# Optimization experiments

Measured on AMD Instinct MI355X. Metric: run time of the kernel, lower is better.

## Reference

```python
import jax, jax.numpy as jnp
import numpy as np

H, W, V = 32, 64, 13
B, C_IN = 8, 256
RADIUS = 6371.0 * 1000.0
NUM_LAT = H + 2
_j = np.arange(1, NUM_LAT - 1, dtype=np.float64)
_LATS = (90.0 - _j * 180.0 / (NUM_LAT - 1)) * np.pi / 180.0  # [32] radians
PIXEL_X = jnp.asarray(2.0 * np.pi * RADIUS * np.cos(_LATS) / W, dtype=jnp.float32).reshape(1, 1, H, 1)
PIXEL_Y = np.float32(np.pi * RADIUS / (H + 1))
_DZ = np.array([50, 50, 50, 50, 50, 75, 100, 100, 100, 125, 112, 75, 75], dtype=np.float32)
PIXEL_Z = jnp.asarray(_DZ).reshape(1, V, 1, 1)
PRESSURE = jnp.asarray([50, 100, 150, 200, 250, 300, 400, 500, 600, 700, 850, 925, 1000], dtype=jnp.float32).reshape(1, V, 1, 1)
M_Z = jnp.asarray(np.tril(np.ones((V, V), dtype=np.float32)) * _DZ[None, :])  # lower-tri integration matrix
LAT_GRID = jnp.asarray(_LATS, dtype=jnp.float32).reshape(1, 1, H, 1)

OMEGA, L_V, R_GAS, C_P, R_D = 7.29e-5, 2.5e6, 8.314, 1005.0, 287.0
DIFF_RATIO, DT, K_H, K_V = 0.05, 300.0, 15.0, 0.1
SIGMA, EMIS, PTHRESH = 5.67e-8, 0.7, 0.8
sg = jax.lax.stop_gradient


def d_x(f):  # periodic 4th-order diff along W, kernel [1,-8,0,8,-1]/12
    g = (jnp.roll(f, 2, 3) - 8.0 * jnp.roll(f, 1, 3) + 8.0 * jnp.roll(f, -1, 3) - jnp.roll(f, -2, 3)) / 12.0
    return g / PIXEL_X


def d_y(f):  # replicate-block padding along H, kernel [-1,8,0,-8,1]/12
    p = jnp.concatenate([f[:, :, :2], f, f[:, :, -2:]], axis=2)
    g = (-p[:, :, :-4] + 8.0 * p[:, :, 1:-3] - 8.0 * p[:, :, 3:-1] + p[:, :, 4:]) / 12.0
    return g / PIXEL_Y


def d_z(f):  # replicate-block padding along level dim (axis 1)
    p = jnp.concatenate([f[:, :2], f, f[:, -2:]], axis=1)
    g = (-p[:, :-4] + 8.0 * p[:, 1:-3] - 8.0 * p[:, 3:-1] + p[:, 4:]) / 12.0
    return g / PIXEL_Z


def integral_z(f):
    return jnp.einsum('ij,bjhw->bihw', M_Z, f)


def conv3x3(x, w, b):
    y = jax.lax.conv_general_dilated(x, w, (1, 1), ((1, 1), (1, 1)), dimension_numbers=('NCHW', 'OIHW', 'NCHW'))
    return y + b[None, :, None, None]


def batchnorm(x, g, b, eps=1e-5):  # training-mode BN (batch statistics)
    m = x.mean(axis=(0, 2, 3), keepdims=True)
    v = x.var(axis=(0, 2, 3), keepdims=True)
    return (x - m) / jnp.sqrt(v + eps) * g.reshape(1, -1, 1, 1) + b.reshape(1, -1, 1, 1)


def scale_tensor(t, a, b):
    mn, mx = sg(t.min()), sg(t.max())
    return (t - mn) / (mx - mn) * (b - a) + a


def scale_diff(d, x):
    mn, me, mx = sg(x.min()), sg(x.mean()), sg(x.max())
    return scale_tensor(d, (mn - me) * DIFF_RATIO, (mx - me) * DIFF_RATIO)


def avoid_inf(t, thr=1.0):
    t = jnp.where(jnp.abs(t) == 0.0, jnp.full_like(t, 0.1), t)
    return jnp.where(jnp.abs(t) < thr, jnp.sign(t) * thr, t)


def mixing(f):
    return K_H * (d_x(d_x(f)) + d_y(d_y(f))) + K_V * d_z(d_z(f))


def rad_cool(t):
    ta = t + 273.15
    return -(EMIS * SIGMA * ta ** 4) / (C_P * PRESSURE * 100.0 / (R_D * ta))


def saturation(t, z_z):
    rho = -1.0 / avoid_inf(z_z)
    p = rho * R_GAS * t
    tc = t - 273.15
    e_s = 6.112 * jnp.exp(scale_tensor(17.67 * tc / avoid_inf(tc + 243.5), -3.47, 3.01)) * 100.0
    return jnp.maximum(0.622 * e_s / avoid_inf(p - 0.378 * e_s), 1e-6)


def precip(q, q_s):
    rh = q / avoid_inf(q_s)
    rate = (rh > PTHRESH).astype(q.dtype) * (q - PTHRESH * q_s) / DT
    return rate, rate * L_V / C_P


def uv_dt(u, v, w, u_x, v_y, z_x, z_y):
    # u_x, v_y are held fixed across RK stages (stateful self.u_x/self.v_y in the original)
    f_cor = 2.0 * OMEGA * jnp.sin(LAT_GRID)
    u_t = -u * u_x - v * d_y(u) - w * d_z(u) + f_cor * v - z_x + mixing(u)
    v_t = -u * d_x(v) - v * v_y - w * d_z(v) - f_cor * u - z_y + mixing(v)
    return u_t, v_t


def t_dt(u, v, w, t, q, q_s, z_z):
    Q = -L_V * z_z * w
    _, lh = precip(q, q_s)
    return (Q - z_z * w) / C_P - u * d_x(t) - v * d_y(t) - w * d_z(t) + mixing(t) + rad_cool(t) + lh


def pde_forward(x, w_norm, b_norm, w_innorm, b_innorm, coef, gz, bz, gq, bq, gu, bu, gv, bv, gt, bt, gblk, bblk):
    h = conv3x3(x, w_norm, b_norm)  # [B, 65, H, W]
    z, q, u, v, t = jnp.split(h, 5, axis=1)
    z = batchnorm(z, gz, bz); q = batchnorm(q, gq, bq)
    u = batchnorm(u, gu, bu); v = batchnorm(v, gv, bv); t = batchnorm(t, gt, bt)
    z_x, z_y, z_z = d_x(z), d_y(z), d_z(z)
    u_x, v_y = d_x(u), d_y(v)
    w_vel = -integral_z(u_x + v_y)  # continuity: dw/dz = -(u_x + v_y)
    # --- RK4 momentum evolution ---
    k1u, k1v = uv_dt(u, v, w_vel, u_x, v_y, z_x, z_y)
    k2u, k2v = uv_dt(u + 0.5 * DT * k1u, v + 0.5 * DT * k1v, w_vel, u_x, v_y, z_x, z_y)
    k3u, k3v = uv_dt(u + 0.5 * DT * k2u, v + 0.5 * DT * k2v, w_vel, u_x, v_y, z_x, z_y)
    k4u, k4v = uv_dt(u + DT * k3u, v + DT * k3v, w_vel, u_x, v_y, z_x, z_y)
    u_new = u + sg(scale_diff((k1u + 2 * k2u + 2 * k3u + k4u) / 6.0 * DT, u))
    v_new = v + sg(scale_diff((k1v + 2 * k2v + 2 * k3v + k4v) / 6.0 * DT, v))
    # --- RK4 temperature evolution (q_s fixed from initial t) ---
    q_s = saturation(t, z_z)
    k1t = t_dt(u, v, w_vel, t, q, q_s, z_z)
    k2t = t_dt(u, v, w_vel, t + 0.5 * DT * k1t, q, q_s, z_z)
    k3t = t_dt(u, v, w_vel, t + 0.5 * DT * k2t, q, q_s, z_z)
    k4t = t_dt(u, v, w_vel, t + DT * k3t, q, q_s, z_z)
    t_new = t + sg(scale_diff((k1t + 2 * k2t + 2 * k3t + k4t) / 6.0 * DT, t))
    # geopotential tendency uses stateful self.t_t (last computed stage = k4t)
    z_t = integral_z(-R_GAS / PRESSURE * k4t)
    z_new = z + sg(scale_diff(z_t * DT, z))
    # moisture evolution
    pr, _ = precip(q, q_s)
    q_t = -u * d_x(q) - v * d_y(q) - w_vel * d_z(q) + mixing(q) - pr
    q_new = q + sg(scale_diff(q_t * DT, q))
    phys = jnp.concatenate([z_new, q_new, u_new, v_new, t_new], axis=1)
    out = coef * phys + (1.0 - coef) * h
    out = conv3x3(out, w_innorm, b_innorm)
    return batchnorm(out, gblk, bblk) + x


def setup_inputs() -> dict:
    key = jax.random.key(0)
    k0, k1, k2 = jax.random.split(key, 3)
    VD = V * 5
    ones13 = jnp.ones((V,), jnp.float32)
    zeros13 = jnp.zeros((V,), jnp.float32)
    return {
        'x': jax.random.normal(k0, (B, C_IN, H, W), jnp.float32),
        'w_norm': jax.random.normal(k1, (VD, C_IN, 3, 3), jnp.float32) * 0.02,
        'b_norm': jnp.zeros((VD,), jnp.float32),
        'w_innorm': jax.random.normal(k2, (C_IN, VD, 3, 3), jnp.float32) * 0.02,
        'b_innorm': jnp.zeros((C_IN,), jnp.float32),
        'coef': 0.5 * jnp.ones((1, VD, H, W), jnp.float32),
        'gz': 0.1 * ones13, 'bz': zeros13,
        'gq': 0.1 * ones13, 'bq': zeros13,
        'gu': 0.1 * ones13, 'bu': zeros13,
        'gv': 0.1 * ones13, 'bv': zeros13,
        'gt': 0.1 * ones13, 'bt': zeros13,
        'gblk': jnp.ones((C_IN,), jnp.float32),
        'bblk': jnp.zeros((C_IN,), jnp.float32),
    }


def reference(x, w_norm, b_norm, w_innorm, b_innorm, coef, gz, bz, gq, bq, gu, bu, gv, bv, gt, bt, gblk, bblk):
    return pde_forward(x, w_norm, b_norm, w_innorm, b_innorm, coef, gz, bz, gq, bq, gu, bu, gv, bv, gt, bt, gblk, bblk)
```

## Files before the change

### kernel.cpp

```cpp
#include <hip/hip_runtime.h>
#include <math.h>

#define DEVFN static __device__ __forceinline__

static constexpr int BB = 8, VV = 13, HH = 32, WW = 64;
static constexpr int NPLANE = HH * WW;
static constexpr int NF = BB * VV * NPLANE;
static constexpr int NHB = BB * 65 * NPLANE;

static constexpr float DT = 300.0f;
static constexpr float KHc = 15.0f, KVc = 0.1f;
static constexpr float OMEGAc = 7.29e-5f;
static constexpr float L_Vc = 2.5e6f;
static constexpr float R_GASc = 8.314f;
static constexpr float C_Pc = 1005.0f;
static constexpr float PTHc = 0.8f;
static constexpr float PYc  = (float)(3.14159265358979323846 * 6371000.0 / 33.0);
static constexpr float PXCc = (float)(2.0 * 3.14159265358979323846 * 6371000.0 / 64.0);
static constexpr float RCCc = (float)(0.7 * 5.67e-8 * 287.0 / (1005.0 * 100.0));
static constexpr float FBIG = 3.402823466e38f;

__constant__ float cDZ[13]  = {50,50,50,50,50,75,100,100,100,125,112,75,75};
__constant__ float cPRS[13] = {50,100,150,200,250,300,400,500,600,700,850,925,1000};

typedef short bf16x8 __attribute__((ext_vector_type(8)));
typedef float f32x4 __attribute__((ext_vector_type(4)));

DEVFN int pmh(int r){ return r < 0 ? r + 2 : (r > HH - 1 ? r - 2 : r); }
DEVFN int pmv(int r){ return r < 0 ? r + 2 : (r > VV - 1 ? r - 2 : r); }
DEVFN float latOf(int h){ return (90.0f - (float)(h + 1) * (180.0f / 33.0f)) * 0.017453292519943295f; }
DEVFN float avoid_inf(float t){
  if (t == 0.0f) t = 0.1f;
  if (fabsf(t) < 1.0f) t = copysignf(1.0f, t);
  return t;
}
DEVFN unsigned short f2bf(float f){
  unsigned u = __float_as_uint(f);
  unsigned r = (u + 0x7fffu + ((u >> 16) & 1u)) >> 16;
  return (unsigned short)r;
}

DEVFN float d_xf(const float* __restrict__ F, int rb, int w, float invpx){
  return (F[rb + ((w + 62) & 63)] - 8.f * F[rb + ((w + 63) & 63)]
        + 8.f * F[rb + ((w + 1) & 63)] - F[rb + ((w + 2) & 63)]) * (1.f / 12.f) * invpx;
}
DEVFN float d_yf(const float* __restrict__ F, int bvbase, int h, int w){
  return (-F[bvbase + pmh(h - 2) * 64 + w] + 8.f * F[bvbase + pmh(h - 1) * 64 + w]
          - 8.f * F[bvbase + pmh(h + 1) * 64 + w] + F[bvbase + pmh(h + 2) * 64 + w]) * (1.f / 12.f) * (1.f / PYc);
}
DEVFN float d_zf(const float* __restrict__ F, int bbase, int v, int hw){
  return (-F[bbase + pmv(v - 2) * 2048 + hw] + 8.f * F[bbase + pmv(v - 1) * 2048 + hw]
          - 8.f * F[bbase + pmv(v + 1) * 2048 + hw] + F[bbase + pmv(v + 2) * 2048 + hw]) * (1.f / 12.f) / cDZ[v];
}
DEVFN float dxxf(const float* __restrict__ F, int rb, int w, float invpx){
  float s = F[rb + ((w + 60) & 63)] - 16.f * F[rb + ((w + 61) & 63)] + 64.f * F[rb + ((w + 62) & 63)]
          + 16.f * F[rb + ((w + 63) & 63)] - 130.f * F[rb + w] + 16.f * F[rb + ((w + 1) & 63)]
          + 64.f * F[rb + ((w + 2) & 63)] - 16.f * F[rb + ((w + 3) & 63)] + F[rb + ((w + 4) & 63)];
  return s * (1.f / 144.f) * invpx * invpx;
}
DEVFN float dyyf(const float* __restrict__ F, int bvbase, int h, int w){
  float g0 = d_yf(F, bvbase, pmh(h - 2), w);
  float g1 = d_yf(F, bvbase, pmh(h - 1), w);
  float g2 = d_yf(F, bvbase, pmh(h + 1), w);
  float g3 = d_yf(F, bvbase, pmh(h + 2), w);
  return (-g0 + 8.f * g1 - 8.f * g2 + g3) * (1.f / 12.f) * (1.f / PYc);
}
DEVFN float dzzf(const float* __restrict__ F, int bbase, int v, int hw){
  float g0 = d_zf(F, bbase, pmv(v - 2), hw);
  float g1 = d_zf(F, bbase, pmv(v - 1), hw);
  float g2 = d_zf(F, bbase, pmv(v + 1), hw);
  float g3 = d_zf(F, bbase, pmv(v + 2), hw);
  return (-g0 + 8.f * g1 - 8.f * g2 + g3) * (1.f / 12.f) / cDZ[v];
}

DEVFN float waveRedSum(float v){ for (int o = 32; o; o >>= 1) v += __shfl_down(v, o, 64); return v; }
DEVFN float waveRedMin(float v){ for (int o = 32; o; o >>= 1) v = fminf(v, __shfl_down(v, o, 64)); return v; }
DEVFN float waveRedMax(float v){ for (int o = 32; o; o >>= 1) v = fmaxf(v, __shfl_down(v, o, 64)); return v; }

template<int OP, int NWV>
static __device__ float blockRedN(float v){
  __shared__ float s[NWV];
  v = OP == 0 ? waveRedSum(v) : OP == 1 ? waveRedMin(v) : waveRedMax(v);
  int lane = threadIdx.x & 63, wid = threadIdx.x >> 6;
  __syncthreads();
  if (lane == 0) s[wid] = v;
  __syncthreads();
  float r = s[0];
  #pragma unroll
  for (int k = 1; k < NWV; ++k)
    r = OP == 0 ? r + s[k] : OP == 1 ? fminf(r, s[k]) : fmaxf(r, s[k]);
  return r;
}

struct GB { const float* g[5]; const float* b[5]; };

__global__ void __launch_bounds__(256) pre_k(const float* __restrict__ x,
    const float* __restrict__ w1, const float* __restrict__ w2,
    unsigned short* __restrict__ XT, unsigned short* __restrict__ wp1,
    unsigned short* __restrict__ wp2)
{
  int blk = blockIdx.x, t = threadIdx.x;
  if (blk < 1024){
    __shared__ float tile[16 * 68];
    int zz = blk >> 8, rem = blk & 255;
    int b = rem >> 5, h = rem & 31;
    for (int p = zz * 4; p < zz * 4 + 4; ++p){
      int cbase = p * 16;
      __syncthreads();
      {
        int cl = t >> 4, w4 = (t & 15) * 4;
        float4 v = *(const float4*)(x + (((size_t)(b * 256 + cbase + cl) * 32 + h) * 64 + w4));
        tile[cl * 68 + w4 + 0] = v.x; tile[cl * 68 + w4 + 1] = v.y;
        tile[cl * 68 + w4 + 2] = v.z; tile[cl * 68 + w4 + 3] = v.w;
      }
      __syncthreads();
      {
        int w = t >> 2, c4 = (t & 3) * 4;
        ushort4 o;
        o.x = f2bf(tile[(c4 + 0) * 68 + w]);
        o.y = f2bf(tile[(c4 + 1) * 68 + w]);
        o.z = f2bf(tile[(c4 + 2) * 68 + w]);
        o.w = f2bf(tile[(c4 + 3) * 68 + w]);
        *(ushort4*)(XT + (((size_t)(b * 32 + h) * 64 + w) * 256 + cbase + c4)) = o;
      }
    }
  } else {
    const int T1 = 9 * 80 * 256;
    const int T2 = 9 * 256 * 96;
    int idx = (blk - 1024) * 256 + t;
    if (idx < T1){
      int dir = idx / (80 * 256);
      int r = idx - dir * (80 * 256);
      int co = r / 256, ci = r - co * 256;
      float v = (co < 65) ? w1[((size_t)(co * 256 + ci)) * 9 + dir] : 0.f;
      wp1[idx] = f2bf(v);
    } else if (idx < T1 + T2){
      int j = idx - T1;
      int dir = j / (256 * 96);
      int r = j - dir * (256 * 96);
      int co = r / 96, ci = r - co * 96;
      float v = (ci < 65) ? w2[((size_t)(co * 65 + ci)) * 9 + dir] : 0.f;
      wp2[j] = f2bf(v);
    }
  }
}

template<int CIT, int CIL, int CO, int COp, int NW, int MF, int SWZ>
__global__ void __launch_bounds__(NW * 64) conv_mfma_k(
    const unsigned short* __restrict__ XT, const unsigned short* __restrict__ Wp,
    const float* __restrict__ bias, float* __restrict__ out, float* __restrict__ bnp)
{
  __shared__ __align__(16) unsigned short Xl[3 * 34 * CIL];
  const int C8 = CIL / 8;
  int tid = threadIdx.x;
  int bx = blockIdx.x, b = blockIdx.y;
  int h = bx >> 1, p0 = (bx & 1) << 5;
  int bh = b * 64 + bx;
  int wid = tid >> 6, lane = tid & 63;
  int l15 = lane & 15, q = lane >> 4;

  f32x4 acc[MF][2];
  #pragma unroll
  for (int mf = 0; mf < MF; ++mf)
    #pragma unroll
    for (int nf = 0; nf < 2; ++nf){ f32x4 z = {0.f, 0.f, 0.f, 0.f}; acc[mf][nf] = z; }

  for (int cp = 0; cp < CIT / CIL; ++cp){
    if (cp) __syncthreads();
    for (int idx = tid; idx < 3 * 34 * C8; idx += NW * 64){
      int r = idx / (34 * C8);
      int rest = idx - r * (34 * C8);
      int j = rest / C8;
      int c8 = rest - j * C8;
      int hh = h + r - 1;
      int gw = p0 - 1 + j;
      uint4 val = make_uint4(0, 0, 0, 0);
      if (hh >= 0 && hh < 32 && gw >= 0 && gw < 64)
        val = *(const uint4*)(XT + (((size_t)(b * 32 + hh) * 64 + gw) * CIT + cp * CIL + c8 * 8));
      int dst = (r * 34 + j) * CIL + ((c8 * 8) ^ ((j & SWZ) << 3));
      *(uint4*)(Xl + dst) = val;
    }
    __syncthreads();

    for (int dir = 0; dir < 9; ++dir){
      int dy = dir / 3, dx = dir - dy * 3;
      #pragma unroll
      for (int kc = 0; kc < CIL / 32; ++kc){
        int kb = kc * 32 + q * 8;
        bf16x8 a[MF];
        #pragma unroll
        for (int mf = 0; mf < MF; ++mf){
          int co = wid * (MF * 16) + mf * 16 + l15;
          a[mf] = *(const bf16x8*)(Wp + ((size_t)(dir * COp + co) * CIT + cp * CIL + kb));
        }
        #pragma unroll
        for (int nf = 0; nf < 2; ++nf){
          int j = nf * 16 + l15 + dx;
          bf16x8 bfrag = *(const bf16x8*)(Xl + ((dy * 34 + j) * CIL + (kb ^ ((j & SWZ) << 3))));
          #pragma unroll
          for (int mf = 0; mf < MF; ++mf)
            acc[mf][nf] = __builtin_amdgcn_mfma_f32_16x16x32_bf16(a[mf], bfrag, acc[mf][nf], 0, 0, 0);
        }
      }
    }
  }
  #pragma unroll
  for (int mf = 0; mf < MF; ++mf){
    #pragma unroll
    for (int r = 0; r < 4; ++r){
      int co = wid * (MF * 16) + mf * 16 + q * 4 + r;
      if (CO != COp && co >= CO) continue;
      float bv = bias[co];
      float sv = 0.f, sq = 0.f;
      #pragma unroll
      for (int nf = 0; nf < 2; ++nf){
        int pix = nf * 16 + l15;
        float val = acc[mf][nf][r] + bv;
        out[(size_t)(b * CO + co) * 2048 + h * 64 + p0 + pix] = val;
        sv += val; sq += val * val;
      }
      #pragma unroll
      for (int off = 8; off; off >>= 1){
        sv += __shfl_xor(sv, off, 16);
        sq += __shfl_xor(sq, off, 16);
      }
      if (l15 == 0){
        bnp[((size_t)co * 512 + bh) * 2]     = sv;
        bnp[((size_t)co * 512 + bh) * 2 + 1] = sq;
      }
    }
  }
}

__global__ void __launch_bounds__(256) prep_k(const float* __restrict__ hb,
  const float* __restrict__ bnp1, GB gb,
  float* __restrict__ Fz, float* __restrict__ Fq, float* __restrict__ Fu,
  float* __restrict__ Fvf, float* __restrict__ Ft,
  float* __restrict__ zx, float* __restrict__ zy, float* __restrict__ zz,
  float* __restrict__ ux, float* __restrict__ vy, float* __restrict__ wv,
  float* __restrict__ partS)
{
  __shared__ float As[65], Bs[65];
  int blk = blockIdx.x, t = threadIdx.x;
  {
    int wvid = t >> 6, lane = t & 63;
    for (int ch = wvid; ch < 65; ch += 4){
      const float4* pp = (const float4*)(bnp1 + (size_t)ch * 1024) + lane * 4;
      float s = 0.f, sq = 0.f;
      #pragma unroll
      for (int k = 0; k < 4; ++k){ float4 v = pp[k]; s += v.x + v.z; sq += v.y + v.w; }
      s = waveRedSum(s); sq = waveRedSum(sq);
      if (!lane){
        float m = s * (1.f / 16384.f);
        float var = sq * (1.f / 16384.f) - m * m;
        float rstd = rsqrtf(var + 1e-5f);
        int f = ch / 13, k = ch - f * 13;
        float g = gb.g[f][k], bbv = gb.b[f][k];
        As[ch] = g * rstd; Bs[ch] = bbv - m * g * rstd;
      }
    }
  }
  __syncthreads();

  int part = blk >> 6;
  int col = ((blk & 63) << 8) | t;
  int b = col >> 11, p = col & 2047, h = p >> 6, w = p & 63;
  int hbase = b * 65 * NPLANE;
  auto hn = [&](int ch, int hh, int ww)->float {
    return hb[hbase + ch * 2048 + hh * 64 + ww] * As[ch] + Bs[ch];
  };
  int fb = (b * 13) * 2048 + p;
  float lat = latOf(h);
  float invpx = 1.0f / (PXCc * cosf(lat));
  int wm2 = (w + 62) & 63, wm1 = (w + 63) & 63, wpl1 = (w + 1) & 63, wpl2 = (w + 2) & 63;
  int hm2 = pmh(h - 2), hm1 = pmh(h - 1), hp1 = pmh(h + 1), hp2 = pmh(h + 2);
  float fmn = FBIG, fmx = -FBIG, fsm = 0.f, smn = FBIG, smx = -FBIG;
  if (part < 5){
    int ch0 = part * 13;
    float c[13];
    #pragma unroll
    for (int v = 0; v < 13; ++v) c[v] = hn(ch0 + v, h, w);
    float* Fdst = part == 0 ? Fz : part == 1 ? Fq : part == 2 ? Fu : part == 3 ? Fvf : Ft;
    #pragma unroll
    for (int v = 0; v < 13; ++v) Fdst[fb + v * 2048] = c[v];
    if (part == 0){
      #pragma unroll
      for (int v = 0; v < 13; ++v){
        zz[fb + v * 2048] = (-c[pmv(v - 2)] + 8.f * c[pmv(v - 1)] - 8.f * c[pmv(v + 1)] + c[pmv(v + 2)]) * (1.f / 12.f) / cDZ[v];
        float zxv = (hn(v, h, wm2) - 8.f * hn(v, h, wm1) + 8.f * hn(v, h, wpl1) - hn(v, h, wpl2)) * (1.f / 12.f) * invpx;
        float zyv = (-hn(v, hm2, w) + 8.f * hn(v, hm1, w) - 8.f * hn(v, hp1, w) + hn(v, hp2, w)) * (1.f / 12.f) * (1.f / PYc);
        zx[fb + v * 2048] = zxv; zy[fb + v * 2048] = zyv;
      }
    }
    if (part == 2){
      #pragma unroll
      for (int v = 0; v < 13; ++v){
        float uxv = (hn(26 + v, h, wm2) - 8.f * hn(26 + v, h, wm1) + 8.f * hn(26 + v, h, wpl1) - hn(26 + v, h, wpl2)) * (1.f / 12.f) * invpx;
        ux[fb + v * 2048] = uxv;
      }
    }
    if (part == 3){
      #pragma unroll
      for (int v = 0; v < 13; ++v){
        float vyv = (-hn(39 + v, hm2, w) + 8.f * hn(39 + v, hm1, w) - 8.f * hn(39 + v, hp1, w) + hn(39 + v, hp2, w)) * (1.f / 12.f) * (1.f / PYc);
        vy[fb + v * 2048] = vyv;
      }
    }
    if (part == 4){
      #pragma unroll
      for (int v = 0; v < 13; ++v){
        float tcc = c[v] - 273.15f;
        float arg = 17.67f * tcc / avoid_inf(tcc + 243.5f);
        smn = fminf(smn, arg); smx = fmaxf(smx, arg);
      }
    }
    #pragma unroll
    for (int v = 0; v < 13; ++v){ fmn = fminf(fmn, c[v]); fmx = fmaxf(fmx, c[v]); fsm += c[v]; }
  } else {
    float cum = 0.f;
    #pragma unroll
    for (int v = 0; v < 13; ++v){
      float uxv = (hn(26 + v, h, wm2) - 8.f * hn(26 + v, h, wm1) + 8.f * hn(26 + v, h, wpl1) - hn(26 + v, h, wpl2)) * (1.f / 12.f) * invpx;
      float vyv = (-hn(39 + v, hm2, w) + 8.f * hn(39 + v, hm1, w) - 8.f * hn(39 + v, hp1, w) + hn(39 + v, hp2, w)) * (1.f / 12.f) * (1.f / PYc);
      cum += cDZ[v] * (uxv + vyv);
      wv[fb + v * 2048] = -cum;
    }
  }
  float* pb = partS + blk * 17;
  float r;
  r = blockRedN<1,4>(smn); if (!t) pb[0] = r;
  r = blockRedN<2,4>(smx); if (!t) pb[1] = r;
  #pragma unroll
  for (int f = 0; f < 5; ++f){
    r = blockRedN<1,4>(part == f ? fmn : FBIG);  if (!t) pb[2 + f * 3] = r;
    r = blockRedN<2,4>(part == f ? fmx : -FBIG); if (!t) pb[3 + f * 3] = r;
    r = blockRedN<0,4>(part == f ? fsm : 0.f);   if (!t) pb[4 + f * 3] = r;
  }
}

template<int STAGE>
__global__ void __launch_bounds__(256) stage_k(
  const float* U, const float* Vf, const float* T,
  const float* Fu, const float* Fvf, const float* Ft, const float* Fq,
  const float* ux, const float* vy, const float* zx, const float* zy,
  const float* wv, const float* zz, const float* partS,
  float* C0, float* prr,
  float* Uo, float* Vo, float* To,
  float* duA, float* dvA, float* dtA, float* k4t, float* qtA,
  float* pduv, float* pdt, float* pqt, float cnext)
{
  float ss = 0.f, off = 0.f;
  if (STAGE == 1){
    int tt = threadIdx.x;
    float v0 = partS[tt * 17], v1 = partS[tt * 17 + 1];
    if (tt < 128){
      v0 = fminf(v0, partS[(tt + 256) * 17]);
      v1 = fmaxf(v1, partS[(tt + 256) * 17 + 1]);
    }
    float smn = blockRedN<1,4>(v0);
    float smx = blockRedN<2,4>(v1);
    ss = (3.01f + 3.47f) / (smx - smn);
    off = -3.47f - smn * ss;
  }
  int i = blockIdx.x * 256 + threadIdx.x;
  int w = i & 63, h = (i >> 6) & 31;
  int bv = i >> 11;
  int v = bv % 13;
  int bvbase = bv * 2048;
  int rb = bvbase + h * 64;
  int bbase = (bv - v) * 2048;
  int hw = h * 64 + w;
  float lat = latOf(h);
  float invpx = 1.0f / (PXCc * cosf(lat));
  float fcor = 2.0f * OMEGAc * sinf(lat);
  float wvi = wv[i];
  float Ui = U[i], Vi = Vf[i], Ti = T[i];
  float Fui = (STAGE == 1) ? Ui : Fu[i];
  float Fvi = (STAGE == 1) ? Vi : Fvf[i];

  float dyU = d_yf(U, bvbase, h, w);
  float dzU = d_zf(U, bbase, v, hw);
  float dxV = d_xf(Vf, rb, w, invpx);
  float dzV = d_zf(Vf, bbase, v, hw);
  float mixU = KHc * (dxxf(U, rb, w, invpx) + dyyf(U, bvbase, h, w)) + KVc * dzzf(U, bbase, v, hw);
  float mixV = KHc * (dxxf(Vf, rb, w, invpx) + dyyf(Vf, bvbase, h, w)) + KVc * dzzf(Vf, bbase, v, hw);
  float ku = -Ui * ux[i] - Vi * dyU - wvi * dzU + fcor * Vi - zx[i] + mixU;
  float kv = -Ui * dxV - Vi * vy[i] - wvi * dzV - fcor * Ui - zy[i] + mixV;

  float C0i;
  if (STAGE == 1){
    float zzi = zz[i], qi = Fq[i];
    float rho = -1.0f / avoid_inf(zzi);
    float p = rho * R_GASc * Ti;
    float tcc = Ti - 273.15f;
    float arg = 17.67f * tcc / avoid_inf(tcc + 243.5f);
    float es = 6.112f * expf(arg * ss + off) * 100.0f;
    float qs = fmaxf(0.622f * es / avoid_inf(p - 0.378f * es), 1e-6f);
    float rh = qi / avoid_inf(qs);
    float rate = (rh > PTHc) ? (qi - PTHc * qs) * (1.0f / DT) : 0.0f;
    prr[i] = rate;
    C0i = -(L_Vc + 1.0f) * zzi * wvi * (1.0f / C_Pc) + rate * (L_Vc / C_Pc);
    C0[i] = C0i;
  } else {
    C0i = C0[i];
  }

  float dxT = d_xf(T, rb, w, invpx);
  float dyT = d_yf(T, bvbase, h, w);
  float dzT = d_zf(T, bbase, v, hw);
  float mixT = KHc * (dxxf(T, rb, w, invpx) + dyyf(T, bvbase, h, w)) + KVc * dzzf(T, bbase, v, hw);
  float ta = Ti + 273.15f;
  float t2 = ta * ta;
  float ta5 = t2 * t2 * ta;
  float rc = -RCCc * ta5 / cPRS[v];
  float kt = C0i - Fui * dxT - Fvi * dyT - wvi * dzT + mixT + rc;

  if (STAGE == 1){ duA[i] = ku; dvA[i] = kv; dtA[i] = kt; }
  else if (STAGE < 4){ duA[i] += 2.f * ku; dvA[i] += 2.f * kv; dtA[i] += 2.f * kt; }
  else {
    float au = duA[i] + ku, av = dvA[i] + kv, at = dtA[i] + kt;
    duA[i] = au; dvA[i] = av; dtA[i] = at; k4t[i] = kt;
    float m0 = blockRedN<1,4>(au), m1 = blockRedN<2,4>(au);
    float m2 = blockRedN<1,4>(av), m3 = blockRedN<2,4>(av);
    float m4 = blockRedN<1,4>(at), m5 = blockRedN<2,4>(at);
    if (!threadIdx.x){
      float* pp = pduv + blockIdx.x * 4;
      pp[0] = m0; pp[1] = m1; pp[2] = m2; pp[3] = m3;
      pdt[blockIdx.x * 2] = m4; pdt[blockIdx.x * 2 + 1] = m5;
    }
  }
  if (STAGE < 4){
    float Fti = (STAGE == 1) ? Ti : Ft[i];
    Uo[i] = Fui + cnext * ku;
    Vo[i] = Fvi + cnext * kv;
    To[i] = Fti + cnext * kt;
  }

  if (STAGE == 2){
    float qtv = -Fui * d_xf(Fq, rb, w, invpx) - Fvi * d_yf(Fq, bvbase, h, w) - wvi * d_zf(Fq, bbase, v, hw)
              + KHc * (dxxf(Fq, rb, w, invpx) + dyyf(Fq, bvbase, h, w)) + KVc * dzzf(Fq, bbase, v, hw) - prr[i];
    qtA[i] = qtv;
    float m0 = blockRedN<1,4>(qtv), m1 = blockRedN<2,4>(qtv);
    if (!threadIdx.x){ pqt[blockIdx.x * 2] = m0; pqt[blockIdx.x * 2 + 1] = m1; }
  }
}

__global__ void __launch_bounds__(64) zt_k(const float* __restrict__ k4t, float* __restrict__ zt, float* __restrict__ pmm)
{
  int col = blockIdx.x * 64 + threadIdx.x;
  int b = col >> 11, p = col & 2047;
  int fb = b * 13 * 2048 + p;
  float cum = 0.f, mn = FBIG, mx = -FBIG;
  #pragma unroll
  for (int v = 0; v < 13; ++v){
    cum += cDZ[v] * (-R_GASc / cPRS[v]) * k4t[fb + v * 2048];
    zt[fb + v * 2048] = cum;
    mn = fminf(mn, cum); mx = fmaxf(mx, cum);
  }
  mn = waveRedMin(mn); mx = waveRedMax(mx);
  if (!threadIdx.x){ pmm[blockIdx.x * 2] = mn; pmm[blockIdx.x * 2 + 1] = mx; }
}

__global__ void __launch_bounds__(256) outmid_fused_k(
  const float* __restrict__ hb,
  const float* __restrict__ Fz, const float* __restrict__ Fq, const float* __restrict__ Fu,
  const float* __restrict__ Fvf, const float* __restrict__ Ft,
  const float* __restrict__ ztA, const float* __restrict__ qtA,
  const float* __restrict__ duA, const float* __restrict__ dvA, const float* __restrict__ dtA,
  const float* __restrict__ coef, const float* __restrict__ partS,
  const float* __restrict__ pduv, const float* __restrict__ pdt,
  const float* __restrict__ pqt, const float* __restrict__ pzt,
  unsigned short* __restrict__ MT)
{
  __shared__ float tileBig[65 * 66];
  int blk = blockIdx.x, t = threadIdx.x;

  float fmn[5] = {FBIG, FBIG, FBIG, FBIG, FBIG};
  float fmx[5] = {-FBIG, -FBIG, -FBIG, -FBIG, -FBIG};
  float fsm[5] = {0.f, 0.f, 0.f, 0.f, 0.f};
  #pragma unroll 1
  for (int r0 = t; r0 < 384; r0 += 256){
    const float* pr = partS + r0 * 17;
    #pragma unroll
    for (int f = 0; f < 5; ++f){
      fmn[f] = fminf(fmn[f], pr[2 + f * 3]);
      fmx[f] = fmaxf(fmx[f], pr[3 + f * 3]);
      fsm[f] += pr[4 + f * 3];
    }
  }
  #pragma unroll
  for (int f = 0; f < 5; ++f){
    fmn[f] = blockRedN<1,4>(fmn[f]);
    fmx[f] = blockRedN<2,4>(fmx[f]);
    fsm[f] = blockRedN<0,4>(fsm[f]);
  }
  float dumn = FBIG, dumx = -FBIG, dvmn = FBIG, dvmx = -FBIG, dtmn = FBIG, dtmx = -FBIG;
  float qmn = FBIG, qmx = -FBIG;
  #pragma unroll 1
  for (int r0 = t; r0 < 832; r0 += 256){
    dumn = fminf(dumn, pduv[r0 * 4]);     dumx = fmaxf(dumx, pduv[r0 * 4 + 1]);
    dvmn = fminf(dvmn, pduv[r0 * 4 + 2]); dvmx = fmaxf(dvmx, pduv[r0 * 4 + 3]);
    dtmn = fminf(dtmn, pdt[r0 * 2]);      dtmx = fmaxf(dtmx, pdt[r0 * 2 + 1]);
    qmn = fminf(qmn, pqt[r0 * 2]);        qmx = fmaxf(qmx, pqt[r0 * 2 + 1]);
  }
  float zmn = pzt[t * 2], zmx = pzt[t * 2 + 1];
  dumn = blockRedN<1,4>(dumn); dumx = blockRedN<2,4>(dumx);
  dvmn = blockRedN<1,4>(dvmn); dvmx = blockRedN<2,4>(dvmx);
  dtmn = blockRedN<1,4>(dtmn); dtmx = blockRedN<2,4>(dtmx);
  qmn = blockRedN<1,4>(qmn);   qmx = blockRedN<2,4>(qmx);
  zmn = blockRedN<1,4>(zmn);   zmx = blockRedN<2,4>(zmx);

  float scf[5], off2[5];
  {
    float rmn[5] = {zmn, qmn, dumn, dvmn, dtmn};
    float rmx[5] = {zmx, qmx, dumx, dvmx, dtmx};
    float cfs[5] = {DT, DT, DT / 6.f, DT / 6.f, DT / 6.f};
    #pragma unroll
    for (int f = 0; f < 5; ++f){
      float mnf = fmn[f], mef = fsm[f] * (1.0f / (float)NF), mxf = fmx[f];
      float aa = (mnf - mef) * 0.05f, b2 = (mxf - mef) * 0.05f;
      float cf = cfs[f];
      float dmn = rmn[f] * cf, dmx = rmx[f] * cf;
      float s = (b2 - aa) / (dmx - dmn);
      scf[f] = s * cf; off2[f] = aa - dmn * s;
    }
  }

  int b = blk >> 5, h = blk & 31;
  #pragma unroll 1
  for (int idx = t; idx < 65 * 64; idx += 256){
    int c = idx >> 6, w = idx & 63;
    int f = c / 13, v = c - f * 13;
    int fi = (b * 13 + v) * 2048 + h * 64 + w;
    const float *Fp, *Rp;
    switch (f){
      case 0: Fp = Fz;  Rp = ztA; break;
      case 1: Fp = Fq;  Rp = qtA; break;
      case 2: Fp = Fu;  Rp = duA; break;
      case 3: Fp = Fvf; Rp = dvA; break;
      default: Fp = Ft; Rp = dtA; break;
    }
    float phys = Fp[fi] + Rp[fi] * scf[f] + off2[f];
    float cf = coef[c * 2048 + h * 64 + w];
    float hbv = hb[((size_t)(b * 65 + c)) * 2048 + h * 64 + w];
    tileBig[c * 66 + w] = cf * phys + (1.0f - cf) * hbv;
  }
  __syncthreads();
  #pragma unroll 1
  for (int ph = 0; ph < 6; ++ph){
    int cbase = ph * 16;
    int w = t >> 2, c4 = (t & 3) * 4;
    int c0 = cbase + c4;
    ushort4 o;
    o.x = (c0 + 0 < 65) ? f2bf(tileBig[(c0 + 0) * 66 + w]) : (unsigned short)0;
    o.y = (c0 + 1 < 65) ? f2bf(tileBig[(c0 + 1) * 66 + w]) : (unsigned short)0;
    o.z = (c0 + 2 < 65) ? f2bf(tileBig[(c0 + 2) * 66 + w]) : (unsigned short)0;
    o.w = (c0 + 3 < 65) ? f2bf(tileBig[(c0 + 3) * 66 + w]) : (unsigned short)0;
    *(ushort4*)(MT + (((size_t)(b * 32 + h) * 64 + w) * 96 + c0)) = o;
  }
}

__global__ void __launch_bounds__(256) final_k(float* __restrict__ y, const float* __restrict__ x,
  const float* __restrict__ bnp2, const float* __restrict__ gblk, const float* __restrict__ bblk)
{
  int blk = blockIdx.x, t = threadIdx.x;
  int c = (blk >> 1) & 255;
  float4 pv = ((const float4*)(bnp2 + (size_t)c * 1024))[t];
  float s = pv.x + pv.z, sq = pv.y + pv.w;
  s = blockRedN<0,4>(s); sq = blockRedN<0,4>(sq);
  float m = s * (1.0f / 16384.0f);
  float var = sq * (1.0f / 16384.0f) - m * m;
  float rstd = rsqrtf(var + 1e-5f);
  float a = gblk[c] * rstd, bb = bblk[c] - m * gblk[c] * rstd;
  int e4 = blk * 256 + t;
  float4 v = ((const float4*)y)[e4];
  float4 xv = ((const float4*)x)[e4];
  v.x = v.x * a + bb + xv.x;
  v.y = v.y * a + bb + xv.y;
  v.z = v.z * a + bb + xv.z;
  v.w = v.w * a + bb + xv.w;
  ((float4*)y)[e4] = v;
}

extern "C" void kernel_launch(void* const* d_in, const int* in_sizes, int n_in,
                              void* d_out, int out_size, void* d_ws, size_t ws_size,
                              hipStream_t stream)
{
  (void)in_sizes; (void)n_in; (void)out_size; (void)ws_size;
  const float* x        = (const float*)d_in[0];
  const float* w_norm   = (const float*)d_in[1];
  const float* b_norm   = (const float*)d_in[2];
  const float* w_innorm = (const float*)d_in[3];
  const float* b_innorm = (const float*)d_in[4];
  const float* coef     = (const float*)d_in[5];
  GB gb;
  for (int f = 0; f < 5; ++f){
    gb.g[f] = (const float*)d_in[6 + 2 * f];
    gb.b[f] = (const float*)d_in[7 + 2 * f];
  }
  const float* gblk = (const float*)d_in[16];
  const float* bblk = (const float*)d_in[17];
  float* yout = (float*)d_out;

  float* ws = (float*)d_ws;
  size_t off = 0;
  auto alloc = [&](size_t n){ float* p = ws + off; off += n; return p; };
  float* hb  = alloc(NHB);
  float* Fz  = alloc(NF); float* Fq  = alloc(NF); float* Fu  = alloc(NF);
  float* Fvf = alloc(NF); float* Ft  = alloc(NF);
  float* zx  = alloc(NF); float* zy  = alloc(NF); float* zz  = alloc(NF);
  float* ux  = alloc(NF); float* vy  = alloc(NF); float* wvel = alloc(NF);
  float* C0  = alloc(NF); float* prr = alloc(NF);
  float* Ua  = alloc(NF); float* Ub  = alloc(NF); float* Va  = alloc(NF); float* Vb = alloc(NF);
  float* Ta  = alloc(NF); float* Tb  = alloc(NF);
  float* duA = alloc(NF); float* dvA = alloc(NF); float* dtA = alloc(NF);
  float* k4t = alloc(NF); float* ztA = alloc(NF); float* qtA = alloc(NF);
  float* part1 = alloc(384 * 17 + 4);
  float* pduv = alloc(832 * 4); float* pdt = alloc(832 * 2);
  float* pqt  = alloc(832 * 2); float* pzt = alloc(256 * 2);
  float* bnp1 = alloc(65 * 512 * 2);
  float* bnp2 = alloc(256 * 512 * 2);
  float* Wp1f = alloc(9 * 80 * 256 / 2);
  float* Wp2f = alloc(9 * 256 * 96 / 2);
  unsigned short* Wp1 = (unsigned short*)Wp1f;
  unsigned short* Wp2 = (unsigned short*)Wp2f;
  unsigned short* XT = (unsigned short*)Ua;
  unsigned short* MT = (unsigned short*)C0;

  pre_k<<<2608, 256, 0, stream>>>(x, w_norm, w_innorm, XT, Wp1, Wp2);
  conv_mfma_k<256, 128, 65, 80, 5, 1, 7><<<dim3(64, 8), 5 * 64, 0, stream>>>(XT, Wp1, b_norm, hb, bnp1);
  prep_k<<<384, 256, 0, stream>>>(hb, bnp1, gb, Fz, Fq, Fu, Fvf, Ft, zx, zy, zz, ux, vy, wvel, part1);
  stage_k<1><<<NF / 256, 256, 0, stream>>>(Fu, Fvf, Ft, Fu, Fvf, Ft, Fq, ux, vy, zx, zy, wvel, zz, part1,
      C0, prr, Ua, Va, Ta, duA, dvA, dtA, k4t, qtA, pduv, pdt, pqt, 0.5f * DT);
  stage_k<2><<<NF / 256, 256, 0, stream>>>(Ua, Va, Ta, Fu, Fvf, Ft, Fq, ux, vy, zx, zy, wvel, zz, part1,
      C0, prr, Ub, Vb, Tb, duA, dvA, dtA, k4t, qtA, pduv, pdt, pqt, 0.5f * DT);
  stage_k<3><<<NF / 256, 256, 0, stream>>>(Ub, Vb, Tb, Fu, Fvf, Ft, Fq, ux, vy, zx, zy, wvel, zz, part1,
      C0, prr, Ua, Va, Ta, duA, dvA, dtA, k4t, qtA, pduv, pdt, pqt, DT);
  stage_k<4><<<NF / 256, 256, 0, stream>>>(Ua, Va, Ta, Fu, Fvf, Ft, Fq, ux, vy, zx, zy, wvel, zz, part1,
      C0, prr, Ub, Vb, Tb, duA, dvA, dtA, k4t, qtA, pduv, pdt, pqt, 0.f);
  zt_k<<<256, 64, 0, stream>>>(k4t, ztA, pzt);
  outmid_fused_k<<<256, 256, 0, stream>>>(hb, Fz, Fq, Fu, Fvf, Ft, ztA, qtA, duA, dvA, dtA,
      coef, part1, pduv, pdt, pqt, pzt, MT);
  conv_mfma_k<96, 96, 256, 256, 8, 2, 3><<<dim3(64, 8), 8 * 64, 0, stream>>>(MT, Wp2, b_innorm, yout, bnp2);
  final_k<<<4096, 256, 0, stream>>>(yout, x, bnp2, gblk, bblk);
}
```

Before: 181.2 us.

## Split RK stage kernel into per-field grid slices and precompute vertical constants

Each RK stage kernel now launches a 2D grid whose y-dimension selects one field (U, V, T, or the q tendency in stage 2). Each block computes only that field's stencils, which gives three to four times as many independent blocks with fewer registers each. The stencil divisions by dz and pressure are replaced with precomputed reciprocal constant tables, and the stage kernel pointers get __restrict__. The trade-off is that the split blocks re-read shared inputs such as U, V, Fu and Fvf, and the float constants may round slightly differently from the original divisions.

```diff
diff --git a/kernel.cpp b/kernel.cpp
--- a/kernel.cpp
+++ b/kernel.cpp
@@ -17,11 +17,25 @@
 static constexpr float PTHc = 0.8f;
 static constexpr float PYc  = (float)(3.14159265358979323846 * 6371000.0 / 33.0);
 static constexpr float PXCc = (float)(2.0 * 3.14159265358979323846 * 6371000.0 / 64.0);
-static constexpr float RCCc = (float)(0.7 * 5.67e-8 * 287.0 / (1005.0 * 100.0));
+static constexpr double RCCd = 0.7 * 5.67e-8 * 287.0 / (1005.0 * 100.0);
 static constexpr float FBIG = 3.402823466e38f;
 
 __constant__ float cDZ[13]  = {50,50,50,50,50,75,100,100,100,125,112,75,75};
-__constant__ float cPRS[13] = {50,100,150,200,250,300,400,500,600,700,850,925,1000};
+__constant__ float cZI[13] = {
+  (float)(1.0/600.0), (float)(1.0/600.0), (float)(1.0/600.0), (float)(1.0/600.0), (float)(1.0/600.0),
+  (float)(1.0/900.0), (float)(1.0/1200.0), (float)(1.0/1200.0), (float)(1.0/1200.0),
+  (float)(1.0/1500.0), (float)(1.0/1344.0), (float)(1.0/900.0), (float)(1.0/900.0)};
+__constant__ float cRC[13] = {
+  (float)(-RCCd/50.0), (float)(-RCCd/100.0), (float)(-RCCd/150.0), (float)(-RCCd/200.0),
+  (float)(-RCCd/250.0), (float)(-RCCd/300.0), (float)(-RCCd/400.0), (float)(-RCCd/500.0),
+  (float)(-RCCd/600.0), (float)(-RCCd/700.0), (float)(-RCCd/850.0), (float)(-RCCd/925.0),
+  (float)(-RCCd/1000.0)};
+__constant__ float cZW[13] = {
+  (float)(50.0*(-8.314/50.0)), (float)(50.0*(-8.314/100.0)), (float)(50.0*(-8.314/150.0)),
+  (float)(50.0*(-8.314/200.0)), (float)(50.0*(-8.314/250.0)), (float)(75.0*(-8.314/300.0)),
+  (float)(100.0*(-8.314/400.0)), (float)(100.0*(-8.314/500.0)), (float)(100.0*(-8.314/600.0)),
+  (float)(125.0*(-8.314/700.0)), (float)(112.0*(-8.314/850.0)), (float)(75.0*(-8.314/925.0)),
+  (float)(75.0*(-8.314/1000.0))};
 
 typedef short bf16x8 __attribute__((ext_vector_type(8)));
 typedef float f32x4 __attribute__((ext_vector_type(4)));
@@ -50,7 +64,7 @@
 }
 DEVFN float d_zf(const float* __restrict__ F, int bbase, int v, int hw){
   return (-F[bbase + pmv(v - 2) * 2048 + hw] + 8.f * F[bbase + pmv(v - 1) * 2048 + hw]
-          - 8.f * F[bbase + pmv(v + 1) * 2048 + hw] + F[bbase + pmv(v + 2) * 2048 + hw]) * (1.f / 12.f) / cDZ[v];
+          - 8.f * F[bbase + pmv(v + 1) * 2048 + hw] + F[bbase + pmv(v + 2) * 2048 + hw]) * cZI[v];
 }
 DEVFN float dxxf(const float* __restrict__ F, int rb, int w, float invpx){
   float s = F[rb + ((w + 60) & 63)] - 16.f * F[rb + ((w + 61) & 63)] + 64.f * F[rb + ((w + 62) & 63)]
@@ -70,7 +84,7 @@
   float g1 = d_zf(F, bbase, pmv(v - 1), hw);
   float g2 = d_zf(F, bbase, pmv(v + 1), hw);
   float g3 = d_zf(F, bbase, pmv(v + 2), hw);
-  return (-g0 + 8.f * g1 - 8.f * g2 + g3) * (1.f / 12.f) / cDZ[v];
+  return (-g0 + 8.f * g1 - 8.f * g2 + g3) * cZI[v];
 }
 
 DEVFN float waveRedSum(float v){ for (int o = 32; o; o >>= 1) v += __shfl_down(v, o, 64); return v; }
@@ -286,7 +300,7 @@
     if (part == 0){
       #pragma unroll
       for (int v = 0; v < 13; ++v){
-        zz[fb + v * 2048] = (-c[pmv(v - 2)] + 8.f * c[pmv(v - 1)] - 8.f * c[pmv(v + 1)] + c[pmv(v + 2)]) * (1.f / 12.f) / cDZ[v];
+        zz[fb + v * 2048] = (-c[pmv(v - 2)] + 8.f * c[pmv(v - 1)] - 8.f * c[pmv(v + 1)] + c[pmv(v + 2)]) * cZI[v];
         float zxv = (hn(v, h, wm2) - 8.f * hn(v, h, wm1) + 8.f * hn(v, h, wpl1) - hn(v, h, wpl2)) * (1.f / 12.f) * invpx;
         float zyv = (-hn(v, hm2, w) + 8.f * hn(v, hm1, w) - 8.f * hn(v, hp1, w) + hn(v, hp2, w)) * (1.f / 12.f) * (1.f / PYc);
         zx[fb + v * 2048] = zxv; zy[fb + v * 2048] = zyv;
@@ -340,29 +354,21 @@
 
 template<int STAGE>
 __global__ void __launch_bounds__(256) stage_k(
-  const float* U, const float* Vf, const float* T,
-  const float* Fu, const float* Fvf, const float* Ft, const float* Fq,
-  const float* ux, const float* vy, const float* zx, const float* zy,
-  const float* wv, const float* zz, const float* partS,
+  const float* __restrict__ U, const float* __restrict__ Vf, const float* __restrict__ T,
+  const float* __restrict__ Fu, const float* __restrict__ Fvf, const float* __restrict__ Ft,
+  const float* __restrict__ Fq,
+  const float* __restrict__ ux, const float* __restrict__ vy,
+  const float* __restrict__ zx, const float* __restrict__ zy,
+  const float* __restrict__ wv, const float* __restrict__ zz,
+  const float* __restrict__ partS,
   float* C0, float* prr,
   float* Uo, float* Vo, float* To,
   float* duA, float* dvA, float* dtA, float* k4t, float* qtA,
   float* pduv, float* pdt, float* pqt, float cnext)
 {
-  float ss = 0.f, off = 0.f;
-  if (STAGE == 1){
-    int tt = threadIdx.x;
-    float v0 = partS[tt * 17], v1 = partS[tt * 17 + 1];
-    if (tt < 128){
-      v0 = fminf(v0, partS[(tt + 256) * 17]);
-      v1 = fmaxf(v1, partS[(tt + 256) * 17 + 1]);
-    }
-    float smn = blockRedN<1,4>(v0);
-    float smx = blockRedN<2,4>(v1);
-    ss = (3.01f + 3.47f) / (smx - smn);
-    off = -3.47f - smn * ss;
-  }
-  int i = blockIdx.x * 256 + threadIdx.x;
+  int part = blockIdx.y;
+  int blk = blockIdx.x, t = threadIdx.x;
+  int i = blk * 256 + t;
   int w = i & 63, h = (i >> 6) & 31;
   int bv = i >> 11;
   int v = bv % 13;
@@ -372,76 +378,94 @@
   int hw = h * 64 + w;
   float lat = latOf(h);
   float invpx = 1.0f / (PXCc * cosf(lat));
-  float fcor = 2.0f * OMEGAc * sinf(lat);
   float wvi = wv[i];
-  float Ui = U[i], Vi = Vf[i], Ti = T[i];
-  float Fui = (STAGE == 1) ? Ui : Fu[i];
-  float Fvi = (STAGE == 1) ? Vi : Fvf[i];
-
-  float dyU = d_yf(U, bvbase, h, w);
-  float dzU = d_zf(U, bbase, v, hw);
-  float dxV = d_xf(Vf, rb, w, invpx);
-  float dzV = d_zf(Vf, bbase, v, hw);
-  float mixU = KHc * (dxxf(U, rb, w, invpx) + dyyf(U, bvbase, h, w)) + KVc * dzzf(U, bbase, v, hw);
-  float mixV = KHc * (dxxf(Vf, rb, w, invpx) + dyyf(Vf, bvbase, h, w)) + KVc * dzzf(Vf, bbase, v, hw);
-  float ku = -Ui * ux[i] - Vi * dyU - wvi * dzU + fcor * Vi - zx[i] + mixU;
-  float kv = -Ui * dxV - Vi * vy[i] - wvi * dzV - fcor * Ui - zy[i] + mixV;
-
-  float C0i;
-  if (STAGE == 1){
-    float zzi = zz[i], qi = Fq[i];
-    float rho = -1.0f / avoid_inf(zzi);
-    float p = rho * R_GASc * Ti;
-    float tcc = Ti - 273.15f;
-    float arg = 17.67f * tcc / avoid_inf(tcc + 243.5f);
-    float es = 6.112f * expf(arg * ss + off) * 100.0f;
-    float qs = fmaxf(0.622f * es / avoid_inf(p - 0.378f * es), 1e-6f);
-    float rh = qi / avoid_inf(qs);
-    float rate = (rh > PTHc) ? (qi - PTHc * qs) * (1.0f / DT) : 0.0f;
-    prr[i] = rate;
-    C0i = -(L_Vc + 1.0f) * zzi * wvi * (1.0f / C_Pc) + rate * (L_Vc / C_Pc);
-    C0[i] = C0i;
-  } else {
-    C0i = C0[i];
-  }
-
-  float dxT = d_xf(T, rb, w, invpx);
-  float dyT = d_yf(T, bvbase, h, w);
-  float dzT = d_zf(T, bbase, v, hw);
-  float mixT = KHc * (dxxf(T, rb, w, invpx) + dyyf(T, bvbase, h, w)) + KVc * dzzf(T, bbase, v, hw);
-  float ta = Ti + 273.15f;
-  float t2 = ta * ta;
-  float ta5 = t2 * t2 * ta;
-  float rc = -RCCc * ta5 / cPRS[v];
-  float kt = C0i - Fui * dxT - Fvi * dyT - wvi * dzT + mixT + rc;
-
-  if (STAGE == 1){ duA[i] = ku; dvA[i] = kv; dtA[i] = kt; }
-  else if (STAGE < 4){ duA[i] += 2.f * ku; dvA[i] += 2.f * kv; dtA[i] += 2.f * kt; }
-  else {
-    float au = duA[i] + ku, av = dvA[i] + kv, at = dtA[i] + kt;
-    duA[i] = au; dvA[i] = av; dtA[i] = at; k4t[i] = kt;
-    float m0 = blockRedN<1,4>(au), m1 = blockRedN<2,4>(au);
-    float m2 = blockRedN<1,4>(av), m3 = blockRedN<2,4>(av);
-    float m4 = blockRedN<1,4>(at), m5 = blockRedN<2,4>(at);
-    if (!threadIdx.x){
-      float* pp = pduv + blockIdx.x * 4;
-      pp[0] = m0; pp[1] = m1; pp[2] = m2; pp[3] = m3;
-      pdt[blockIdx.x * 2] = m4; pdt[blockIdx.x * 2 + 1] = m5;
-    }
-  }
-  if (STAGE < 4){
-    float Fti = (STAGE == 1) ? Ti : Ft[i];
-    Uo[i] = Fui + cnext * ku;
-    Vo[i] = Fvi + cnext * kv;
-    To[i] = Fti + cnext * kt;
-  }
-
-  if (STAGE == 2){
+
+  if (part == 0){
+    float Ui = U[i], Vi = Vf[i];
+    float fcor = 2.0f * OMEGAc * sinf(lat);
+    float dyU = d_yf(U, bvbase, h, w);
+    float dzU = d_zf(U, bbase, v, hw);
+    float mixU = KHc * (dxxf(U, rb, w, invpx) + dyyf(U, bvbase, h, w)) + KVc * dzzf(U, bbase, v, hw);
+    float ku = -Ui * ux[i] - Vi * dyU - wvi * dzU + fcor * Vi - zx[i] + mixU;
+    if (STAGE == 1) duA[i] = ku;
+    else if (STAGE < 4) duA[i] += 2.f * ku;
+    else {
+      float au = duA[i] + ku; duA[i] = au;
+      float m0 = blockRedN<1,4>(au), m1 = blockRedN<2,4>(au);
+      if (!t){ pduv[blk * 4] = m0; pduv[blk * 4 + 1] = m1; }
+    }
+    if (STAGE < 4) Uo[i] = Fu[i] + cnext * ku;
+  } else if (part == 1){
+    float Ui = U[i], Vi = Vf[i];
+    float fcor = 2.0f * OMEGAc * sinf(lat);
+    float dxV = d_xf(Vf, rb, w, invpx);
+    float dzV = d_zf(Vf, bbase, v, hw);
+    float mixV = KHc * (dxxf(Vf, rb, w, invpx) + dyyf(Vf, bvbase, h, w)) + KVc * dzzf(Vf, bbase, v, hw);
+    float kv = -Ui * dxV - Vi * vy[i] - wvi * dzV - fcor * Ui - zy[i] + mixV;
+    if (STAGE == 1) dvA[i] = kv;
+    else if (STAGE < 4) dvA[i] += 2.f * kv;
+    else {
+      float av = dvA[i] + kv; dvA[i] = av;
+      float m2 = blockRedN<1,4>(av), m3 = blockRedN<2,4>(av);
+      if (!t){ pduv[blk * 4 + 2] = m2; pduv[blk * 4 + 3] = m3; }
+    }
+    if (STAGE < 4) Vo[i] = Fvf[i] + cnext * kv;
+  } else if (part == 2){
+    float ss = 0.f, off = 0.f;
+    if (STAGE == 1){
+      float v0 = partS[t * 17], v1 = partS[t * 17 + 1];
+      if (t < 128){
+        v0 = fminf(v0, partS[(t + 256) * 17]);
+        v1 = fmaxf(v1, partS[(t + 256) * 17 + 1]);
+      }
+      float smn = blockRedN<1,4>(v0);
+      float smx = blockRedN<2,4>(v1);
+      ss = (3.01f + 3.47f) / (smx - smn);
+      off = -3.47f - smn * ss;
+    }
+    float Ti = T[i];
+    float Fui = Fu[i], Fvi = Fvf[i];
+    float C0i;
+    if (STAGE == 1){
+      float zzi = zz[i], qi = Fq[i];
+      float rho = -1.0f / avoid_inf(zzi);
+      float p = rho * R_GASc * Ti;
+      float tcc = Ti - 273.15f;
+      float arg = 17.67f * tcc / avoid_inf(tcc + 243.5f);
+      float es = 6.112f * expf(arg * ss + off) * 100.0f;
+      float qs = fmaxf(0.622f * es / avoid_inf(p - 0.378f * es), 1e-6f);
+      float rh = qi / avoid_inf(qs);
+      float rate = (rh > PTHc) ? (qi - PTHc * qs) * (1.0f / DT) : 0.0f;
+      prr[i] = rate;
+      C0i = -(L_Vc + 1.0f) * zzi * wvi * (1.0f / C_Pc) + rate * (L_Vc / C_Pc);
+      C0[i] = C0i;
+    } else {
+      C0i = C0[i];
+    }
+    float dxT = d_xf(T, rb, w, invpx);
+    float dyT = d_yf(T, bvbase, h, w);
+    float dzT = d_zf(T, bbase, v, hw);
+    float mixT = KHc * (dxxf(T, rb, w, invpx) + dyyf(T, bvbase, h, w)) + KVc * dzzf(T, bbase, v, hw);
+    float ta = Ti + 273.15f;
+    float t2 = ta * ta;
+    float ta5 = t2 * t2 * ta;
+    float rc = cRC[v] * ta5;
+    float kt = C0i - Fui * dxT - Fvi * dyT - wvi * dzT + mixT + rc;
+    if (STAGE == 1) dtA[i] = kt;
+    else if (STAGE < 4) dtA[i] += 2.f * kt;
+    else {
+      float at = dtA[i] + kt; dtA[i] = at; k4t[i] = kt;
+      float m4 = blockRedN<1,4>(at), m5 = blockRedN<2,4>(at);
+      if (!t){ pdt[blk * 2] = m4; pdt[blk * 2 + 1] = m5; }
+    }
+    if (STAGE < 4) To[i] = Ft[i] + cnext * kt;
+  } else if (STAGE == 2){
+    float Fui = Fu[i], Fvi = Fvf[i];
     float qtv = -Fui * d_xf(Fq, rb, w, invpx) - Fvi * d_yf(Fq, bvbase, h, w) - wvi * d_zf(Fq, bbase, v, hw)
               + KHc * (dxxf(Fq, rb, w, invpx) + dyyf(Fq, bvbase, h, w)) + KVc * dzzf(Fq, bbase, v, hw) - prr[i];
     qtA[i] = qtv;
     float m0 = blockRedN<1,4>(qtv), m1 = blockRedN<2,4>(qtv);
-    if (!threadIdx.x){ pqt[blockIdx.x * 2] = m0; pqt[blockIdx.x * 2 + 1] = m1; }
+    if (!t){ pqt[blk * 2] = m0; pqt[blk * 2 + 1] = m1; }
   }
 }
 
@@ -453,7 +477,7 @@
   float cum = 0.f, mn = FBIG, mx = -FBIG;
   #pragma unroll
   for (int v = 0; v < 13; ++v){
-    cum += cDZ[v] * (-R_GASc / cPRS[v]) * k4t[fb + v * 2048];
+    cum += cZW[v] * k4t[fb + v * 2048];
     zt[fb + v * 2048] = cum;
     mn = fminf(mn, cum); mx = fmaxf(mx, cum);
   }
@@ -630,13 +654,13 @@
   pre_k<<<2608, 256, 0, stream>>>(x, w_norm, w_innorm, XT, Wp1, Wp2);
   conv_mfma_k<256, 128, 65, 80, 5, 1, 7><<<dim3(64, 8), 5 * 64, 0, stream>>>(XT, Wp1, b_norm, hb, bnp1);
   prep_k<<<384, 256, 0, stream>>>(hb, bnp1, gb, Fz, Fq, Fu, Fvf, Ft, zx, zy, zz, ux, vy, wvel, part1);
-  stage_k<1><<<NF / 256, 256, 0, stream>>>(Fu, Fvf, Ft, Fu, Fvf, Ft, Fq, ux, vy, zx, zy, wvel, zz, part1,
+  stage_k<1><<<dim3(NF / 256, 3), 256, 0, stream>>>(Fu, Fvf, Ft, Fu, Fvf, Ft, Fq, ux, vy, zx, zy, wvel, zz, part1,
       C0, prr, Ua, Va, Ta, duA, dvA, dtA, k4t, qtA, pduv, pdt, pqt, 0.5f * DT);
-  stage_k<2><<<NF / 256, 256, 0, stream>>>(Ua, Va, Ta, Fu, Fvf, Ft, Fq, ux, vy, zx, zy, wvel, zz, part1,
+  stage_k<2><<<dim3(NF / 256, 4), 256, 0, stream>>>(Ua, Va, Ta, Fu, Fvf, Ft, Fq, ux, vy, zx, zy, wvel, zz, part1,
       C0, prr, Ub, Vb, Tb, duA, dvA, dtA, k4t, qtA, pduv, pdt, pqt, 0.5f * DT);
-  stage_k<3><<<NF / 256, 256, 0, stream>>>(Ub, Vb, Tb, Fu, Fvf, Ft, Fq, ux, vy, zx, zy, wvel, zz, part1,
+  stage_k<3><<<dim3(NF / 256, 3), 256, 0, stream>>>(Ub, Vb, Tb, Fu, Fvf, Ft, Fq, ux, vy, zx, zy, wvel, zz, part1,
       C0, prr, Ua, Va, Ta, duA, dvA, dtA, k4t, qtA, pduv, pdt, pqt, DT);
-  stage_k<4><<<NF / 256, 256, 0, stream>>>(Ua, Va, Ta, Fu, Fvf, Ft, Fq, ux, vy, zx, zy, wvel, zz, part1,
+  stage_k<4><<<dim3(NF / 256, 3), 256, 0, stream>>>(Ua, Va, Ta, Fu, Fvf, Ft, Fq, ux, vy, zx, zy, wvel, zz, part1,
       C0, prr, Ub, Vb, Tb, duA, dvA, dtA, k4t, qtA, pduv, pdt, pqt, 0.f);
   zt_k<<<256, 64, 0, stream>>>(k4t, ztA, pzt);
   outmid_fused_k<<<256, 256, 0, stream>>>(hb, Fz, Fq, Fu, Fvf, Ft, ztA, qtA, duA, dvA, dtA,
```

Result: slower. 189.4 us (+4.5%).
